# Optimization experiments

Hardware: AMD Instinct MI355X
Metric: run time of the kernel (lower is better)

The kernel has to match this reference:

```python
import jax, jax.numpy as jnp
import numpy as np

N_ENT, N_USR, C, E, NNZ, NREL, NHOPS = 150000, 60000, 64, 1000000, 1000000, 10, 2
EPS = 1e-12  # torch F.normalize default eps


def setup_inputs() -> dict:
    key = jax.random.key(0)
    ks = jax.random.split(key, 8)
    return {
        "user_emb": jax.random.normal(ks[0], (N_USR, C), dtype=jnp.float32),
        "entity_emb": jax.random.normal(ks[1], (N_ENT, C), dtype=jnp.float32),
        "weight": jax.random.normal(ks[2], (NREL - 1, C), dtype=jnp.float32) * 0.1,  # xavier-ish
        "inter_vals": jax.random.uniform(ks[3], (NNZ,), dtype=jnp.float32),
        "edge_index": jax.random.randint(ks[4], (2, E), 0, N_ENT),
        "edge_type": jax.random.randint(ks[5], (E,), 0, NREL - 1),
        "inter_rows": jax.random.randint(ks[6], (NNZ,), 0, N_USR),
        "inter_cols": jax.random.randint(ks[7], (NNZ,), 0, N_ENT),
    }


def _l2_normalize(x):
    n = jnp.sqrt(jnp.sum(x * x, axis=1, keepdims=True))
    return x / jnp.maximum(n, EPS)


def _hop(entity_emb, user_emb, head, tail, edge_type, weight,
         inter_rows, inter_cols, inter_vals):
    rel = weight[edge_type - 1]                      # [E, C]
    h = entity_emb[head]                             # [E, C]
    t = entity_emb[tail]                             # [E, C]
    neigh = t * rel                                  # [E, C]
    # calculate_sim_hrt: (||h*r||_2 * ||t*r||_2)^2, per-edge scalar
    hn = jnp.linalg.norm(h * rel, axis=1)            # [E]
    tn = jnp.linalg.norm(t * rel, axis=1)            # [E]
    att = (hn * tn) ** 2                             # [E]
    # scatter_softmax over groups of `head` (value identical across channels)
    m = jax.ops.segment_max(att, head, num_segments=N_ENT)
    e = jnp.exp(att - m[head])
    s = jax.ops.segment_sum(e, head, num_segments=N_ENT)
    w = e / s[head]                                  # [E]
    entity_agg = jax.ops.segment_sum(w[:, None] * neigh, head, num_segments=N_ENT)
    # entity_agg += interact_mat.T @ user_emb
    entity_agg = entity_agg + jax.ops.segment_sum(
        inter_vals[:, None] * user_emb[inter_rows], inter_cols, num_segments=N_ENT)
    # user_agg = interact_mat @ entity_emb
    user_agg = jax.ops.segment_sum(
        inter_vals[:, None] * entity_emb[inter_cols], inter_rows, num_segments=N_USR)
    return entity_agg, user_agg


def reference(user_emb, entity_emb, weight, inter_vals,
              edge_index, edge_type, inter_rows, inter_cols):
    head, tail = edge_index[0], edge_index[1]
    ent_res, usr_res = entity_emb, user_emb
    ent, usr = entity_emb, user_emb
    for _ in range(NHOPS):
        ent, usr = _hop(ent, usr, head, tail, edge_type, weight,
                        inter_rows, inter_cols, inter_vals)
        ent = _l2_normalize(ent)  # mess_dropout disabled (eval path)
        usr = _l2_normalize(usr)
        ent_res = ent_res + ent
        usr_res = usr_res + usr
    return ent_res, usr_res
```

## Files before the change

### kernel.cpp

```cpp
#include <hip/hip_runtime.h>
#include <hip/hip_fp16.h>
#include <math.h>

#define N_ENT  150000
#define N_USR  60000
#define CDIM   64
#define NE     1000000
#define NNZV   1000000
#define NREL9  9
#define NTOT   (2 * N_ENT + N_USR)
#define TOTAL_ITEMS (NE + 2 * NNZV)
#define SCAN_B ((NTOT + 1023) / 1024)

#define NXCD   8
#define H_PER  (N_ENT / NXCD)
#define R_PER  (N_USR / NXCD)
#define EPB    2048
#define NCHUNK ((NE + EPB - 1) / EPB)

#define EG (N_ENT / 4)
#define UG (N_USR / 4)

template <int CTRL>
__device__ __forceinline__ float dpp_addf(float v) {
    int iv = __float_as_int(v);
    int x = __builtin_amdgcn_update_dpp(iv, iv, CTRL, 0xF, 0xF, true);
    return v + __int_as_float(x);
}
template <int CTRL>
__device__ __forceinline__ float dpp_maxf(float v) {
    int iv = __float_as_int(v);
    int x = __builtin_amdgcn_update_dpp(iv, iv, CTRL, 0xF, 0xF, true);
    return fmaxf(v, __int_as_float(x));
}
__device__ __forceinline__ float wave_sum(float v) {
    v = dpp_addf<0x111>(v);
    v = dpp_addf<0x112>(v);
    v = dpp_addf<0x114>(v);
    v = dpp_addf<0x118>(v);
    v = dpp_addf<0x142>(v);
    v = dpp_addf<0x143>(v);
    return __int_as_float(__builtin_amdgcn_readlane(__float_as_int(v), 63));
}
__device__ __forceinline__ float wave_max(float v) {
    v = dpp_maxf<0x111>(v);
    v = dpp_maxf<0x112>(v);
    v = dpp_maxf<0x114>(v);
    v = dpp_maxf<0x118>(v);
    v = dpp_maxf<0x142>(v);
    v = dpp_maxf<0x143>(v);
    return __int_as_float(__builtin_amdgcn_readlane(__float_as_int(v), 63));
}

__device__ __forceinline__ int   bcast_i(int v, int l)   { return __builtin_amdgcn_readlane(v, l); }
__device__ __forceinline__ float bcast_f(float v, int l) { return __int_as_float(__builtin_amdgcn_readlane(__float_as_int(v), l)); }

__device__ __forceinline__ int block_excl_scan(int v, int* lds) {
    int lane = threadIdx.x & 63, wid = threadIdx.x >> 6;
    int incl = v;
#pragma unroll
    for (int o = 1; o < 64; o <<= 1) {
        int t = __shfl_up(incl, o, 64);
        if (lane >= o) incl += t;
    }
    if (lane == 63) lds[wid] = incl;
    __syncthreads();
    int nw = blockDim.x >> 6;
    if ((int)threadIdx.x < nw) {
        int s = lds[threadIdx.x];
        int si = s;
        for (int o = 1; o < nw; o <<= 1) {
            int t = __shfl_up(si, o, 64);
            if ((int)threadIdx.x >= o) si += t;
        }
        lds[threadIdx.x] = si - s;
    }
    __syncthreads();
    return incl - v + lds[wid];
}

__global__ __launch_bounds__(256) void k_zero(int* __restrict__ p, int n) {
    int i = blockIdx.x * 256 + threadIdx.x;
    if (i < n) p[i] = 0;
}

__global__ __launch_bounds__(256) void k_cvt(
    const float* __restrict__ src, __half* __restrict__ dst, int n2)
{
    int i = blockIdx.x * 256 + threadIdx.x;
    if (i >= n2) return;
    float2 v = ((const float2*)src)[i];
    ((__half2*)dst)[i] = __floats2half2_rn(v.x, v.y);
}


__global__ __launch_bounds__(256) void k_hist(
    const int* __restrict__ head, const int* __restrict__ cols,
    const int* __restrict__ rows, int* __restrict__ cnt)
{
    int i = blockIdx.x * 256 + threadIdx.x;
    if (i >= NE) return;
    atomicAdd(cnt + head[i], 1);
    atomicAdd(cnt + N_ENT + cols[i], 1);
    atomicAdd(cnt + 2 * N_ENT + rows[i], 1);
}

__global__ __launch_bounds__(1024) void k_bsum(
    const int* __restrict__ cnt, int* __restrict__ bsum)
{
    __shared__ int lds[16];
    int i = blockIdx.x * 1024 + threadIdx.x;
    float v = (i < NTOT) ? (float)cnt[i] : 0.f;
    float s = wave_sum(v);
    int lane = threadIdx.x & 63, wid = threadIdx.x >> 6;
    if (lane == 0) lds[wid] = (int)s;
    __syncthreads();
    if (threadIdx.x == 0) {
        int t = 0;
        for (int k = 0; k < 16; ++k) t += lds[k];
        bsum[blockIdx.x] = t;
    }
}

__global__ __launch_bounds__(512) void k_scan_small(int* __restrict__ bsum)
{
    __shared__ int lds[16];
    int i = threadIdx.x;
    int v = (i < SCAN_B) ? bsum[i] : 0;
    int e = block_excl_scan(v, lds);
    if (i < SCAN_B) bsum[i] = e;
}

__global__ __launch_bounds__(1024) void k_scan_apply(
    const int* __restrict__ cnt, const int* __restrict__ bsum,
    int* __restrict__ start, int* __restrict__ cursor)
{
    __shared__ int lds[16];
    int i = blockIdx.x * 1024 + threadIdx.x;
    int v = (i < NTOT) ? cnt[i] : 0;
    int e = block_excl_scan(v, lds) + bsum[blockIdx.x];
    if (i < NTOT) { start[i] = e; cursor[i] = e; }
    else if (i == NTOT) { start[i] = TOTAL_ITEMS; }
}

__global__ __launch_bounds__(256) void k_scatter(
    const int* __restrict__ head, const int* __restrict__ tail,
    const int* __restrict__ etype,
    const int* __restrict__ rows, const int* __restrict__ cols,
    const float* __restrict__ vals,
    int* __restrict__ cursor,
    int* __restrict__ pk_h,
    int2* __restrict__ rc,
    int2* __restrict__ cv)
{
    int role  = blockIdx.x & (NXCD - 1);
    int chunk = blockIdx.x >> 3;
    int h0 = role * H_PER, h1 = h0 + H_PER;
    int r0 = role * R_PER, r1 = r0 + R_PER;
    int base = chunk * EPB;
    int end  = min(base + EPB, NE);
    for (int i = base + (int)threadIdx.x; i < end; i += 256) {
        int h = head[i];
        int c = cols[i];
        int r = rows[i];
        if (h >= h0 && h < h1) {
            int rt = etype[i] - 1;
            if (rt < 0) rt = 8;
            int p = atomicAdd(cursor + h, 1);
            if ((unsigned)p < (unsigned)NE) pk_h[p] = tail[i] | (rt << 18);
        }
        if (c >= h0 && c < h1) {
            int vb = __float_as_int(vals[i]);
            int p = atomicAdd(cursor + N_ENT + c, 1) - NE;
            if ((unsigned)p < (unsigned)NNZV) rc[p] = make_int2(r, vb);
        }
        if (r >= r0 && r < r1) {
            int vb = __float_as_int(vals[i]);
            int p = atomicAdd(cursor + 2 * N_ENT + r, 1) - 2 * NE;
            if ((unsigned)p < (unsigned)NNZV) cv[p] = make_int2(c, vb);
        }
    }
}

__global__ __launch_bounds__(256) void k_sqnorm(
    const float* __restrict__ ent_cur, const float* __restrict__ wt,
    float* __restrict__ sq)
{
    int e = (blockIdx.x * 256 + threadIdx.x) >> 6;
    int lane = threadIdx.x & 63;
    if (e >= N_ENT) return;
    float own = ent_cur[(e << 6) + lane];
    float o2 = own * own;
    float mine = 0.f;
#pragma unroll
    for (int rt = 0; rt < NREL9; ++rt) {
        float r = wt[(rt << 6) + lane];
        float s = wave_sum(o2 * r * r);
        if (lane == rt) mine = s;
    }
    if (lane < NREL9) sq[e * NREL9 + lane] = mine;
}

template <bool FIRST, bool LAST>
__global__ __launch_bounds__(256) void k_hop(
    const __half* __restrict__ ent16_cur, const __half* __restrict__ usr16_cur,
    const float* __restrict__ ent_res_base, const float* __restrict__ usr_res_base,
    const float* __restrict__ wt, const int* __restrict__ start,
    const int* __restrict__ pk_h, const float* __restrict__ sq_in,
    const int2* __restrict__ rc, const int2* __restrict__ cv,
    __half* __restrict__ ent16_next, __half* __restrict__ usr16_next,
    float* __restrict__ sq_out,
    float* __restrict__ out_ent, float* __restrict__ out_usr)
{
    int lane = threadIdx.x & 63;
    int b = blockIdx.x;

    if (b < EG) {
        int e = (b * 256 + (int)threadIdx.x) >> 6;

        int s1 = min(start[e + 1], NE);
        int s0 = min(start[e], s1);
        float m = 0.f, l = 0.f, acc = 0.f;
        for (int base = s0; base < s1; base += 64) {
            int j = base + lane;
            int cnt = min(64, s1 - base);
            int pk = 0; float att = 0.f;
            if (j < s1) {
                pk = pk_h[j];
                int t = pk & 0x3FFFF, rt = (pk >> 18) & 15;
                att = sq_in[e * NREL9 + rt] * sq_in[t * NREL9 + rt];
            }
            float mn = fmaxf(m, wave_max(att));
            float scale = __expf(m - mn);
            float p = (j < s1) ? __expf(att - mn) : 0.f;
            l = l * scale + wave_sum(p);
            acc *= scale;
            m = mn;
            int k = 0;
            for (; k + 4 <= cnt; k += 4) {
#pragma unroll
                for (int q = 0; q < 4; ++q) {
                    int pkk = bcast_i(pk, k + q);
                    float wk = bcast_f(p, k + q);
                    const __half* tp = ent16_cur + ((pkk & 0x3FFFF) << 6);
                    const float*  wp = wt + (((pkk >> 18) & 15) << 6);
                    acc += wk * __half2float(tp[lane]) * wp[lane];
                }
            }
            for (; k < cnt; ++k) {
                int pkk = bcast_i(pk, k);
                float wk = bcast_f(p, k);
                const __half* tp = ent16_cur + ((pkk & 0x3FFFF) << 6);
                const float*  wp = wt + (((pkk >> 18) & 15) << 6);
                acc += wk * __half2float(tp[lane]) * wp[lane];
            }
        }
        float agg = (l > 0.f) ? acc / l : 0.f;

        int c1 = min(start[N_ENT + e + 1] - NE, NNZV);
        int c0 = max(min(start[N_ENT + e] - NE, c1), 0);
        for (int base = c0; base < c1; base += 64) {
            int j = base + lane;
            int cnt = min(64, c1 - base);
            int rr = 0; float vv = 0.f;
            if (j < c1) { int2 q = rc[j]; rr = q.x; vv = __int_as_float(q.y); }
            int k = 0;
            for (; k + 4 <= cnt; k += 4) {
#pragma unroll
                for (int q = 0; q < 4; ++q) {
                    int u = bcast_i(rr, k + q);
                    float v = bcast_f(vv, k + q);
                    agg += v * __half2float(usr16_cur[(u << 6) + lane]);
                }
            }
            for (; k < cnt; ++k) {
                int u = bcast_i(rr, k);
                float v = bcast_f(vv, k);
                agg += v * __half2float(usr16_cur[(u << 6) + lane]);
            }
        }

        float s = wave_sum(agg * agg);
        float y = agg / fmaxf(sqrtf(s), 1e-12f);
        int oi = (e << 6) + lane;
        if (!LAST) {
            ent16_next[oi] = __float2half(y);
            float y2 = y * y;
            float mine = 0.f;
#pragma unroll
            for (int rt = 0; rt < NREL9; ++rt) {
                float r = wt[(rt << 6) + lane];
                float sv = wave_sum(y2 * r * r);
                if (lane == rt) mine = sv;
            }
            if (lane < NREL9) sq_out[e * NREL9 + lane] = mine;
        }
        if (FIRST) out_ent[oi] = ent_res_base[oi] + y;
        else       out_ent[oi] += y;
    } else {
        int u = ((b - EG) * 256 + (int)threadIdx.x) >> 6;
        int s1 = min(start[2 * N_ENT + u + 1] - 2 * NE, NNZV);
        int s0 = max(min(start[2 * N_ENT + u] - 2 * NE, s1), 0);
        float acc = 0.f;
        for (int base = s0; base < s1; base += 64) {
            int j = base + lane;
            int cnt = min(64, s1 - base);
            int cc = 0; float vv = 0.f;
            if (j < s1) { int2 q = cv[j]; cc = q.x; vv = __int_as_float(q.y); }
            int k = 0;
            for (; k + 4 <= cnt; k += 4) {
#pragma unroll
                for (int q = 0; q < 4; ++q) {
                    int c = bcast_i(cc, k + q);
                    float v = bcast_f(vv, k + q);
                    acc += v * __half2float(ent16_cur[(c << 6) + lane]);
                }
            }
            for (; k < cnt; ++k) {
                int c = bcast_i(cc, k);
                float v = bcast_f(vv, k);
                acc += v * __half2float(ent16_cur[(c << 6) + lane]);
            }
        }
        float s = wave_sum(acc * acc);
        float y = acc / fmaxf(sqrtf(s), 1e-12f);
        int oi = (u << 6) + lane;
        if (!LAST) usr16_next[oi] = __float2half(y);
        if (FIRST) out_usr[oi] = usr_res_base[oi] + y;
        else       out_usr[oi] += y;
    }
}

extern "C" void kernel_launch(void* const* d_in, const int* in_sizes, int n_in,
                              void* d_out, int out_size, void* d_ws, size_t ws_size,
                              hipStream_t stream)
{
    const float* user_emb   = (const float*)d_in[0];
    const float* entity_emb = (const float*)d_in[1];
    const float* wt         = (const float*)d_in[2];
    const float* inter_vals = (const float*)d_in[3];
    const int*   edge_index = (const int*)d_in[4];
    const int*   etype      = (const int*)d_in[5];
    const int*   inter_rows = (const int*)d_in[6];
    const int*   inter_cols = (const int*)d_in[7];
    const int* head  = edge_index;
    const int* tailp = edge_index + NE;

    __half* ent16_a = (__half*)d_ws;
    __half* ent16_b = ent16_a + (size_t)N_ENT * CDIM;
    __half* usr16_a = ent16_b + (size_t)N_ENT * CDIM;
    __half* usr16_b = usr16_a + (size_t)N_USR * CDIM;
    int2*  rc     = (int2*)(usr16_b + (size_t)N_USR * CDIM);
    int2*  cv     = rc + NNZV;
    int*   pk_h   = (int*)(cv + NNZV);
    int*   cnt    = pk_h + NE;
    int*   start  = cnt + NTOT;
    int*   cursor = start + NTOT + 1;
    int*   bsum   = cursor + NTOT + 1;
    float* sq_a   = (float*)(bsum + SCAN_B);
    float* sq_b   = sq_a + (size_t)N_ENT * NREL9;

    float* out_ent = (float*)d_out;
    float* out_usr = out_ent + (size_t)N_ENT * CDIM;

    {
        int n2e = N_ENT * CDIM / 2, n2u = N_USR * CDIM / 2;
        k_cvt<<<(n2e + 255) / 256, 256, 0, stream>>>(entity_emb, ent16_a, n2e);
        k_cvt<<<(n2u + 255) / 256, 256, 0, stream>>>(user_emb, usr16_a, n2u);
    }

    k_zero<<<(NTOT + 255) / 256, 256, 0, stream>>>(cnt, NTOT);
    k_hist<<<(NE + 255) / 256, 256, 0, stream>>>(head, inter_cols, inter_rows, cnt);
    k_bsum<<<SCAN_B, 1024, 0, stream>>>(cnt, bsum);
    k_scan_small<<<1, 512, 0, stream>>>(bsum);
    k_scan_apply<<<SCAN_B, 1024, 0, stream>>>(cnt, bsum, start, cursor);
    k_scatter<<<NCHUNK * NXCD, 256, 0, stream>>>(
        head, tailp, etype, inter_rows, inter_cols, inter_vals,
        cursor, pk_h, rc, cv);

    k_sqnorm<<<EG, 256, 0, stream>>>(entity_emb, wt, sq_a);
    k_hop<true, false><<<EG + UG, 256, 0, stream>>>(
        ent16_a, usr16_a, entity_emb, user_emb, wt, start, pk_h, sq_a, rc, cv,
        ent16_b, usr16_b, sq_b, out_ent, out_usr);

    k_hop<false, true><<<EG + UG, 256, 0, stream>>>(
        ent16_b, usr16_b, nullptr, nullptr, wt, start, pk_h, sq_b, rc, cv,
        nullptr, nullptr, nullptr, out_ent, out_usr);
}
```

Measured before the change: 712.5 us.

## Sort head edges by relation so relation weight multiplies once per segment

The CSR for head edges is now keyed by (head, relation), so each head's edges are grouped by relation type. The aggregation loop accumulates weighted tail embeddings per relation and multiplies by the relation weight once per group, removing a per-edge weight load and multiply. Other changes: the entity fp16 conversion is fused into the squared-norm kernel, and workspace buffers (cnt, cursor) are aliased onto sq_a and ent16_b. The scan grows to about 1.56M entries with a two-per-thread top-level scan, adding branchy segment-boundary tracking inside the inner loop.

```diff
diff --git a/kernel.cpp b/kernel.cpp
--- a/kernel.cpp
+++ b/kernel.cpp
@@ -8,9 +8,10 @@
 #define NE     1000000
 #define NNZV   1000000
 #define NREL9  9
-#define NTOT   (2 * N_ENT + N_USR)
+#define E9OFF  (N_ENT * NREL9)
+#define NTOT2  (E9OFF + N_ENT + N_USR)
 #define TOTAL_ITEMS (NE + 2 * NNZV)
-#define SCAN_B ((NTOT + 1023) / 1024)
+#define SCAN_B2 (((NTOT2 + 1) + 1023) / 1024)
 
 #define NXCD   8
 #define H_PER  (N_ENT / NXCD)
@@ -95,14 +96,17 @@
 
 
 __global__ __launch_bounds__(256) void k_hist(
-    const int* __restrict__ head, const int* __restrict__ cols,
-    const int* __restrict__ rows, int* __restrict__ cnt)
+    const int* __restrict__ head, const int* __restrict__ etype,
+    const int* __restrict__ cols, const int* __restrict__ rows,
+    int* __restrict__ cnt)
 {
     int i = blockIdx.x * 256 + threadIdx.x;
     if (i >= NE) return;
-    atomicAdd(cnt + head[i], 1);
-    atomicAdd(cnt + N_ENT + cols[i], 1);
-    atomicAdd(cnt + 2 * N_ENT + rows[i], 1);
+    int rt = etype[i] - 1;
+    if (rt < 0) rt = 8;
+    atomicAdd(cnt + head[i] * NREL9 + rt, 1);
+    atomicAdd(cnt + E9OFF + cols[i], 1);
+    atomicAdd(cnt + E9OFF + N_ENT + rows[i], 1);
 }
 
 __global__ __launch_bounds__(1024) void k_bsum(
@@ -110,7 +114,7 @@
 {
     __shared__ int lds[16];
     int i = blockIdx.x * 1024 + threadIdx.x;
-    float v = (i < NTOT) ? (float)cnt[i] : 0.f;
+    float v = (i < NTOT2) ? (float)cnt[i] : 0.f;
     float s = wave_sum(v);
     int lane = threadIdx.x & 63, wid = threadIdx.x >> 6;
     if (lane == 0) lds[wid] = (int)s;
@@ -122,13 +126,16 @@
     }
 }
 
-__global__ __launch_bounds__(512) void k_scan_small(int* __restrict__ bsum)
+__global__ __launch_bounds__(1024) void k_scan_small(int* __restrict__ bsum)
 {
     __shared__ int lds[16];
-    int i = threadIdx.x;
-    int v = (i < SCAN_B) ? bsum[i] : 0;
-    int e = block_excl_scan(v, lds);
-    if (i < SCAN_B) bsum[i] = e;
+    int t = threadIdx.x;
+    int i0 = 2 * t, i1 = 2 * t + 1;
+    int a = (i0 < SCAN_B2) ? bsum[i0] : 0;
+    int b = (i1 < SCAN_B2) ? bsum[i1] : 0;
+    int e = block_excl_scan(a + b, lds);
+    if (i0 < SCAN_B2) bsum[i0] = e;
+    if (i1 < SCAN_B2) bsum[i1] = e + a;
 }
 
 __global__ __launch_bounds__(1024) void k_scan_apply(
@@ -137,10 +144,10 @@
 {
     __shared__ int lds[16];
     int i = blockIdx.x * 1024 + threadIdx.x;
-    int v = (i < NTOT) ? cnt[i] : 0;
+    int v = (i < NTOT2) ? cnt[i] : 0;
     int e = block_excl_scan(v, lds) + bsum[blockIdx.x];
-    if (i < NTOT) { start[i] = e; cursor[i] = e; }
-    else if (i == NTOT) { start[i] = TOTAL_ITEMS; }
+    if (i < NTOT2) { start[i] = e; cursor[i] = e; }
+    else if (i == NTOT2) { start[i] = TOTAL_ITEMS; }
 }
 
 __global__ __launch_bounds__(256) void k_scatter(
@@ -166,30 +173,31 @@
         if (h >= h0 && h < h1) {
             int rt = etype[i] - 1;
             if (rt < 0) rt = 8;
-            int p = atomicAdd(cursor + h, 1);
+            int p = atomicAdd(cursor + h * NREL9 + rt, 1);
             if ((unsigned)p < (unsigned)NE) pk_h[p] = tail[i] | (rt << 18);
         }
         if (c >= h0 && c < h1) {
             int vb = __float_as_int(vals[i]);
-            int p = atomicAdd(cursor + N_ENT + c, 1) - NE;
+            int p = atomicAdd(cursor + E9OFF + c, 1) - NE;
             if ((unsigned)p < (unsigned)NNZV) rc[p] = make_int2(r, vb);
         }
         if (r >= r0 && r < r1) {
             int vb = __float_as_int(vals[i]);
-            int p = atomicAdd(cursor + 2 * N_ENT + r, 1) - 2 * NE;
+            int p = atomicAdd(cursor + E9OFF + N_ENT + r, 1) - 2 * NE;
             if ((unsigned)p < (unsigned)NNZV) cv[p] = make_int2(c, vb);
         }
     }
 }
 
-__global__ __launch_bounds__(256) void k_sqnorm(
-    const float* __restrict__ ent_cur, const float* __restrict__ wt,
-    float* __restrict__ sq)
+__global__ __launch_bounds__(256) void k_prep_ent(
+    const float* __restrict__ ent, const float* __restrict__ wt,
+    __half* __restrict__ ent16, float* __restrict__ sq)
 {
     int e = (blockIdx.x * 256 + threadIdx.x) >> 6;
     int lane = threadIdx.x & 63;
     if (e >= N_ENT) return;
-    float own = ent_cur[(e << 6) + lane];
+    float own = ent[(e << 6) + lane];
+    ent16[(e << 6) + lane] = __float2half(own);
     float o2 = own * own;
     float mine = 0.f;
 #pragma unroll
@@ -217,10 +225,13 @@
 
     if (b < EG) {
         int e = (b * 256 + (int)threadIdx.x) >> 6;
-
-        int s1 = min(start[e + 1], NE);
-        int s0 = min(start[e], s1);
+        const int* startp = start + e * NREL9;
+
+        int s1 = min(startp[NREL9], NE);
+        int s0 = min(startp[0], s1);
         float m = 0.f, l = 0.f, acc = 0.f;
+        float racc = 0.f, wv = 0.f;
+        int r_cur = -1, rend = s0;
         for (int base = s0; base < s1; base += 64) {
             int j = base + lane;
             int cnt = min(64, s1 - base);
@@ -235,30 +246,49 @@
             float p = (j < s1) ? __expf(att - mn) : 0.f;
             l = l * scale + wave_sum(p);
             acc *= scale;
+            racc *= scale;
             m = mn;
             int k = 0;
             for (; k + 4 <= cnt; k += 4) {
+                int p0 = bcast_i(pk, k + 0), p1 = bcast_i(pk, k + 1);
+                int p2 = bcast_i(pk, k + 2), p3 = bcast_i(pk, k + 3);
+                float t0 = __half2float(ent16_cur[((p0 & 0x3FFFF) << 6) + lane]);
+                float t1 = __half2float(ent16_cur[((p1 & 0x3FFFF) << 6) + lane]);
+                float t2 = __half2float(ent16_cur[((p2 & 0x3FFFF) << 6) + lane]);
+                float t3 = __half2float(ent16_cur[((p3 & 0x3FFFF) << 6) + lane]);
+                float w0 = bcast_f(p, k + 0), w1 = bcast_f(p, k + 1);
+                float w2 = bcast_f(p, k + 2), w3 = bcast_f(p, k + 3);
 #pragma unroll
                 for (int q = 0; q < 4; ++q) {
-                    int pkk = bcast_i(pk, k + q);
-                    float wk = bcast_f(p, k + q);
-                    const __half* tp = ent16_cur + ((pkk & 0x3FFFF) << 6);
-                    const float*  wp = wt + (((pkk >> 18) & 15) << 6);
-                    acc += wk * __half2float(tp[lane]) * wp[lane];
+                    int ja = base + k + q;
+                    if (ja >= rend) {
+                        acc = fmaf(wv, racc, acc); racc = 0.f;
+                        do { ++r_cur; rend = startp[r_cur + 1]; } while (ja >= rend);
+                        wv = wt[(r_cur << 6) + lane];
+                    }
+                    float tq = (q == 0) ? t0 : (q == 1) ? t1 : (q == 2) ? t2 : t3;
+                    float wq = (q == 0) ? w0 : (q == 1) ? w1 : (q == 2) ? w2 : w3;
+                    racc = fmaf(wq, tq, racc);
                 }
             }
             for (; k < cnt; ++k) {
                 int pkk = bcast_i(pk, k);
                 float wk = bcast_f(p, k);
-                const __half* tp = ent16_cur + ((pkk & 0x3FFFF) << 6);
-                const float*  wp = wt + (((pkk >> 18) & 15) << 6);
-                acc += wk * __half2float(tp[lane]) * wp[lane];
-            }
-        }
+                float tq = __half2float(ent16_cur[((pkk & 0x3FFFF) << 6) + lane]);
+                int ja = base + k;
+                if (ja >= rend) {
+                    acc = fmaf(wv, racc, acc); racc = 0.f;
+                    do { ++r_cur; rend = startp[r_cur + 1]; } while (ja >= rend);
+                    wv = wt[(r_cur << 6) + lane];
+                }
+                racc = fmaf(wk, tq, racc);
+            }
+        }
+        acc = fmaf(wv, racc, acc);
         float agg = (l > 0.f) ? acc / l : 0.f;
 
-        int c1 = min(start[N_ENT + e + 1] - NE, NNZV);
-        int c0 = max(min(start[N_ENT + e] - NE, c1), 0);
+        int c1 = min(start[E9OFF + e + 1] - NE, NNZV);
+        int c0 = max(min(start[E9OFF + e] - NE, c1), 0);
         for (int base = c0; base < c1; base += 64) {
             int j = base + lane;
             int cnt = min(64, c1 - base);
@@ -299,8 +329,8 @@
         else       out_ent[oi] += y;
     } else {
         int u = ((b - EG) * 256 + (int)threadIdx.x) >> 6;
-        int s1 = min(start[2 * N_ENT + u + 1] - 2 * NE, NNZV);
-        int s0 = max(min(start[2 * N_ENT + u] - 2 * NE, s1), 0);
+        int s1 = min(start[E9OFF + N_ENT + u + 1] - 2 * NE, NNZV);
+        int s0 = max(min(start[E9OFF + N_ENT + u] - 2 * NE, s1), 0);
         float acc = 0.f;
         for (int base = s0; base < s1; base += 64) {
             int j = base + lane;
@@ -346,39 +376,39 @@
     const int* head  = edge_index;
     const int* tailp = edge_index + NE;
 
-    __half* ent16_a = (__half*)d_ws;
-    __half* ent16_b = ent16_a + (size_t)N_ENT * CDIM;
-    __half* usr16_a = ent16_b + (size_t)N_ENT * CDIM;
-    __half* usr16_b = usr16_a + (size_t)N_USR * CDIM;
-    int2*  rc     = (int2*)(usr16_b + (size_t)N_USR * CDIM);
-    int2*  cv     = rc + NNZV;
-    int*   pk_h   = (int*)(cv + NNZV);
-    int*   cnt    = pk_h + NE;
-    int*   start  = cnt + NTOT;
-    int*   cursor = start + NTOT + 1;
-    int*   bsum   = cursor + NTOT + 1;
-    float* sq_a   = (float*)(bsum + SCAN_B);
-    float* sq_b   = sq_a + (size_t)N_ENT * NREL9;
+    char* w = (char*)d_ws;
+    __half* ent16_a = (__half*)w;                      w += (size_t)N_ENT * CDIM * 2;
+    __half* ent16_b = (__half*)w;                      w += (size_t)N_ENT * CDIM * 2;
+    __half* usr16_a = (__half*)w;                      w += (size_t)N_USR * CDIM * 2;
+    __half* usr16_b = (__half*)w;                      w += (size_t)N_USR * CDIM * 2;
+    int2*  rc    = (int2*)w;                           w += (size_t)NNZV * 8;
+    int2*  cv    = (int2*)w;                           w += (size_t)NNZV * 8;
+    int*   pk_h  = (int*)w;                            w += (size_t)NE * 4;
+    int*   start = (int*)w;                            w += (size_t)(NTOT2 + 2) * 4;
+    int*   bsum  = (int*)w;                            w += (size_t)SCAN_B2 * 4;
+    float* sq_a  = (float*)w;                          w += (size_t)N_ENT * NREL9 * 4;
+    float* sq_b  = (float*)w;                          w += (size_t)N_ENT * NREL9 * 4;
+    int* cnt    = (int*)sq_a;
+    int* cursor = (int*)ent16_b;
 
     float* out_ent = (float*)d_out;
     float* out_usr = out_ent + (size_t)N_ENT * CDIM;
 
-    {
-        int n2e = N_ENT * CDIM / 2, n2u = N_USR * CDIM / 2;
-        k_cvt<<<(n2e + 255) / 256, 256, 0, stream>>>(entity_emb, ent16_a, n2e);
-        k_cvt<<<(n2u + 255) / 256, 256, 0, stream>>>(user_emb, usr16_a, n2u);
-    }
-
-    k_zero<<<(NTOT + 255) / 256, 256, 0, stream>>>(cnt, NTOT);
-    k_hist<<<(NE + 255) / 256, 256, 0, stream>>>(head, inter_cols, inter_rows, cnt);
-    k_bsum<<<SCAN_B, 1024, 0, stream>>>(cnt, bsum);
-    k_scan_small<<<1, 512, 0, stream>>>(bsum);
-    k_scan_apply<<<SCAN_B, 1024, 0, stream>>>(cnt, bsum, start, cursor);
+    k_zero<<<(NTOT2 + 255) / 256, 256, 0, stream>>>(cnt, NTOT2);
+    k_hist<<<(NE + 255) / 256, 256, 0, stream>>>(head, etype, inter_cols, inter_rows, cnt);
+    k_bsum<<<SCAN_B2, 1024, 0, stream>>>(cnt, bsum);
+    k_scan_small<<<1, 1024, 0, stream>>>(bsum);
+    k_scan_apply<<<SCAN_B2, 1024, 0, stream>>>(cnt, bsum, start, cursor);
     k_scatter<<<NCHUNK * NXCD, 256, 0, stream>>>(
         head, tailp, etype, inter_rows, inter_cols, inter_vals,
         cursor, pk_h, rc, cv);
 
-    k_sqnorm<<<EG, 256, 0, stream>>>(entity_emb, wt, sq_a);
+    k_prep_ent<<<EG, 256, 0, stream>>>(entity_emb, wt, ent16_a, sq_a);
+    {
+        int n2u = N_USR * CDIM / 2;
+        k_cvt<<<(n2u + 255) / 256, 256, 0, stream>>>(user_emb, usr16_a, n2u);
+    }
+
     k_hop<true, false><<<EG + UG, 256, 0, stream>>>(
         ent16_a, usr16_a, entity_emb, user_emb, wt, start, pk_h, sq_a, rc, cv,
         ent16_b, usr16_b, sq_b, out_ent, out_usr);
```

Result: slower. 800.7 us (+12.4%).

## Fuse fp16 conversion into sqnorm prep and XCD-partition histogram atomics

Applied to the files above, without the earlier changes.

The two standalone fp32-to-fp16 conversion kernels are folded into the squared-norm kernel, so entity embeddings are read once to produce both the half copy and the per-relation norms, and user conversion runs in extra blocks of the same launch. The histogram kernel now uses the same XCD-role chunking as the scatter kernel, so each block only does atomics for ids in its partition. The aim is fewer launches, less duplicate reading, and atomics that stay local to one XCD's L2. The cost is that every block reads each chunk of indices eight times.

```diff
diff --git a/kernel.cpp b/kernel.cpp
--- a/kernel.cpp
+++ b/kernel.cpp
@@ -20,6 +20,7 @@
 
 #define EG (N_ENT / 4)
 #define UG (N_USR / 4)
+#define UCVT ((N_USR * CDIM / 2 + 255) / 256)
 
 template <int CTRL>
 __device__ __forceinline__ float dpp_addf(float v) {
@@ -84,25 +85,25 @@
     if (i < n) p[i] = 0;
 }
 
-__global__ __launch_bounds__(256) void k_cvt(
-    const float* __restrict__ src, __half* __restrict__ dst, int n2)
-{
-    int i = blockIdx.x * 256 + threadIdx.x;
-    if (i >= n2) return;
-    float2 v = ((const float2*)src)[i];
-    ((__half2*)dst)[i] = __floats2half2_rn(v.x, v.y);
-}
-
 
 __global__ __launch_bounds__(256) void k_hist(
     const int* __restrict__ head, const int* __restrict__ cols,
     const int* __restrict__ rows, int* __restrict__ cnt)
 {
-    int i = blockIdx.x * 256 + threadIdx.x;
-    if (i >= NE) return;
-    atomicAdd(cnt + head[i], 1);
-    atomicAdd(cnt + N_ENT + cols[i], 1);
-    atomicAdd(cnt + 2 * N_ENT + rows[i], 1);
+    int role  = blockIdx.x & (NXCD - 1);
+    int chunk = blockIdx.x >> 3;
+    int h0 = role * H_PER, h1 = h0 + H_PER;
+    int r0 = role * R_PER, r1 = r0 + R_PER;
+    int base = chunk * EPB;
+    int end  = min(base + EPB, NE);
+    for (int i = base + (int)threadIdx.x; i < end; i += 256) {
+        int h = head[i];
+        int c = cols[i];
+        int r = rows[i];
+        if (h >= h0 && h < h1) atomicAdd(cnt + h, 1);
+        if (c >= h0 && c < h1) atomicAdd(cnt + N_ENT + c, 1);
+        if (r >= r0 && r < r1) atomicAdd(cnt + 2 * N_ENT + r, 1);
+    }
 }
 
 __global__ __launch_bounds__(1024) void k_bsum(
@@ -182,23 +183,34 @@
     }
 }
 
-__global__ __launch_bounds__(256) void k_sqnorm(
-    const float* __restrict__ ent_cur, const float* __restrict__ wt,
+__global__ __launch_bounds__(256) void k_prep(
+    const float* __restrict__ ent, const float* __restrict__ usr,
+    const float* __restrict__ wt,
+    __half* __restrict__ ent16, __half* __restrict__ usr16,
     float* __restrict__ sq)
 {
-    int e = (blockIdx.x * 256 + threadIdx.x) >> 6;
-    int lane = threadIdx.x & 63;
-    if (e >= N_ENT) return;
-    float own = ent_cur[(e << 6) + lane];
-    float o2 = own * own;
-    float mine = 0.f;
-#pragma unroll
-    for (int rt = 0; rt < NREL9; ++rt) {
-        float r = wt[(rt << 6) + lane];
-        float s = wave_sum(o2 * r * r);
-        if (lane == rt) mine = s;
-    }
-    if (lane < NREL9) sq[e * NREL9 + lane] = mine;
+    int b = blockIdx.x;
+    if (b < EG) {
+        int e = (b * 256 + (int)threadIdx.x) >> 6;
+        int lane = threadIdx.x & 63;
+        float own = ent[(e << 6) + lane];
+        ent16[(e << 6) + lane] = __float2half(own);
+        float o2 = own * own;
+        float mine = 0.f;
+#pragma unroll
+        for (int rt = 0; rt < NREL9; ++rt) {
+            float r = wt[(rt << 6) + lane];
+            float s = wave_sum(o2 * r * r);
+            if (lane == rt) mine = s;
+        }
+        if (lane < NREL9) sq[e * NREL9 + lane] = mine;
+    } else {
+        int i = (b - EG) * 256 + (int)threadIdx.x;
+        if (i < N_USR * CDIM / 2) {
+            float2 v = ((const float2*)usr)[i];
+            ((__half2*)usr16)[i] = __floats2half2_rn(v.x, v.y);
+        }
+    }
 }
 
 template <bool FIRST, bool LAST>
@@ -363,14 +375,8 @@
     float* out_ent = (float*)d_out;
     float* out_usr = out_ent + (size_t)N_ENT * CDIM;
 
-    {
-        int n2e = N_ENT * CDIM / 2, n2u = N_USR * CDIM / 2;
-        k_cvt<<<(n2e + 255) / 256, 256, 0, stream>>>(entity_emb, ent16_a, n2e);
-        k_cvt<<<(n2u + 255) / 256, 256, 0, stream>>>(user_emb, usr16_a, n2u);
-    }
-
     k_zero<<<(NTOT + 255) / 256, 256, 0, stream>>>(cnt, NTOT);
-    k_hist<<<(NE + 255) / 256, 256, 0, stream>>>(head, inter_cols, inter_rows, cnt);
+    k_hist<<<NCHUNK * NXCD, 256, 0, stream>>>(head, inter_cols, inter_rows, cnt);
     k_bsum<<<SCAN_B, 1024, 0, stream>>>(cnt, bsum);
     k_scan_small<<<1, 512, 0, stream>>>(bsum);
     k_scan_apply<<<SCAN_B, 1024, 0, stream>>>(cnt, bsum, start, cursor);
@@ -378,7 +384,9 @@
         head, tailp, etype, inter_rows, inter_cols, inter_vals,
         cursor, pk_h, rc, cv);
 
-    k_sqnorm<<<EG, 256, 0, stream>>>(entity_emb, wt, sq_a);
+    k_prep<<<EG + UCVT, 256, 0, stream>>>(
+        entity_emb, user_emb, wt, ent16_a, usr16_a, sq_a);
+
     k_hop<true, false><<<EG + UG, 256, 0, stream>>>(
         ent16_a, usr16_a, entity_emb, user_emb, wt, start, pk_h, sq_a, rc, cv,
         ent16_b, usr16_b, sq_b, out_ent, out_usr);
```

New measurement: 700.8 us. About the same (-1.6%).
